# Performance work log

Hardware: AMD Instinct MI355X
Metric: run time of the kernel (lower is better)

Reference implementation:

```python
import jax, jax.numpy as jnp
import numpy as np

MODEL_W, MODEL_H = 1280.0, 768.0
SCALE = 80.0
NUM_CLASSES = 2


def _decode(pred_boxes):
    # pred_boxes: (bs, 4, H, W) -> decoded xywh box per reference point, (bs, H, W, 4)
    bs, _, H, W = pred_boxes.shape
    p = jnp.transpose(pred_boxes, (0, 2, 3, 1))
    sx = MODEL_W / W
    sy = MODEL_H / H
    rx = (jnp.arange(W, dtype=p.dtype) * sx + sx / 2)[None, None, :]
    ry = (jnp.arange(H, dtype=p.dtype) * sy + sy / 2)[None, :, None]
    x1 = p[..., 0] * SCALE + rx
    y1 = p[..., 1] * SCALE + ry
    x2 = p[..., 2] * SCALE + rx
    y2 = p[..., 3] * SCALE + ry
    w = x2 - x1
    h = y2 - y1
    cx = x1 + w / 2
    cy = y1 + h / 2
    return jnp.stack([cx, cy, w, h], axis=-1)


def _iou_xywh(pred, box):
    # pred: (H, W, 4) xywh, box: (4,) xywh -> (H, W)
    p_min = pred[..., :2] - pred[..., 2:4] / 2
    p_max = pred[..., :2] + pred[..., 2:4] / 2
    b_min = box[:2] - box[2:4] / 2
    b_max = box[:2] + box[2:4] / 2
    imin = jnp.maximum(p_min, b_min)
    imax = jnp.minimum(p_max, b_max)
    iwh = jnp.maximum(imax - imin, 0.0)
    inter = iwh[..., 0] * iwh[..., 1]
    union = pred[..., 2] * pred[..., 3] + box[2] * box[3] - inter
    return inter / jnp.clip(union, 1e-6)


def _assign_image(pred_dec, boxes):
    # pred_dec: (H, W, 4) decoded xywh; boxes: (N, 6) = x1,y1,x2,y2,class_id,extra
    H, W = pred_dec.shape[0], pred_dec.shape[1]
    row = jnp.arange(H, dtype=pred_dec.dtype)[:, None]
    col = jnp.arange(W, dtype=pred_dec.dtype)[None, :]
    cls0 = jnp.concatenate([jnp.ones((H, W, 1), jnp.float32),
                            jnp.zeros((H, W, NUM_CLASSES - 1), jnp.float32)], -1)
    pts0 = jnp.ones((H, W, 6), jnp.float32)
    best0 = jnp.zeros((H, W), jnp.float32)  # best==0 <=> position not yet assigned

    def step(carry, b):
        cls_map, pts_map, best = carry
        x1, y1, x2, y2, cid_f, extra = b[0], b[1], b[2], b[3], b[4], b[5]
        w = x2 - x1
        h = y2 - y1
        cx = x1 + w / 2
        cy = y1 + h / 2
        valid = (w * h) > 0  # original skips zero-area boxes
        box = jnp.stack([cx, cy, w, h])
        iou = _iou_xywh(pred_dec, box)
        # min_max_ref_point_index: rectangle of reference points covered by the box
        miw = jnp.floor(jnp.maximum((cx - w / 2) * W / MODEL_W - 0.5, 0.0))
        mih = jnp.floor(jnp.maximum((cy - h / 2) * H / MODEL_H - 0.5, 0.0))
        maw = jnp.ceil(jnp.minimum((cx + w / 2) * W / MODEL_W - 0.5, W - 1.0))
        mah = jnp.ceil(jnp.minimum((cy + h / 2) * H / MODEL_H - 0.5, H - 1.0))
        rect = (col >= miw) & (col <= maw) & (row >= mih) & (row <= mah) & valid
        iou_f = jnp.where(rect, iou, 0.0)
        # dynamic_k = ceil(max(sum_iou, 1)); keep strictly-top-k ious inside rect
        k = jnp.ceil(jnp.maximum(jnp.sum(iou_f), 1.0)).astype(jnp.int32)
        sorted_desc = -jnp.sort(-iou_f.ravel())
        thresh = jnp.take(sorted_desc, jnp.minimum(k, H * W - 1))  # (k+1)-th largest
        iou_k = jnp.where(iou_f > thresh, iou_f, 0.0)
        lam = jax.lax.rsqrt(k.astype(jnp.float32))
        positive = rect & (iou_k > 0)
        new = positive & (iou_k > best)                 # claim position (incl. unassigned)
        tie = positive & (iou_k == best) & (best > 0)   # equal iou -> zero all classes
        bg = rect & ~(iou_k > 0)                        # inside rect, not positive -> bg=0
        cid = jnp.clip(cid_f.astype(jnp.int32), 0, NUM_CLASSES - 2)
        onehot = jax.nn.one_hot(cid + 1, NUM_CLASSES, dtype=jnp.float32)
        cls_map = jnp.where(new[..., None], onehot, cls_map)
        cls_map = jnp.where(tie[..., None], 0.0, cls_map)
        cls_map = cls_map.at[..., 0].set(jnp.where(bg, 0.0, cls_map[..., 0]))
        pvec = jnp.stack([cx, cy, w, h, extra, lam])
        pts_map = jnp.where(new[..., None], pvec, pts_map)
        best = jnp.where(new, iou_k, best)
        return (cls_map, pts_map, best), None

    (cls_map, pts_map, _), _ = jax.lax.scan(step, (cls0, pts0, best0), boxes)
    return cls_map, pts_map


def setup_inputs():
    key = jax.random.key(0)
    k1, k2, k3, k4, k5, k6, k7 = jax.random.split(key, 7)
    bs, H, W, N = 16, 384, 640, 32
    pred_feat = jax.random.normal(k1, (bs, 3, H, W), dtype=jnp.float32)
    pred_boxes = jax.random.normal(k2, (bs, 4, H, W), dtype=jnp.float32)
    # GT boxes in x1,y1,x2,y2,class_id,extra format (module converts to xywh)
    cx = jax.random.uniform(k3, (bs, N), minval=0.0, maxval=MODEL_W)
    cy = jax.random.uniform(k4, (bs, N), minval=0.0, maxval=MODEL_H)
    w = jax.random.uniform(k5, (bs, N), minval=10.0, maxval=160.0)
    h = jax.random.uniform(k6, (bs, N), minval=10.0, maxval=120.0)
    cid = jnp.zeros((bs, N), jnp.float32)  # num_classes=2 -> single foreground class 0
    extra = jax.random.uniform(k7, (bs, N))
    bboxes = jnp.stack([cx - w / 2, cy - h / 2, cx + w / 2, cy + h / 2, cid, extra],
                       axis=-1).astype(jnp.float32)
    return {"pred_feat": pred_feat, "pred_boxes": pred_boxes, "bboxes": bboxes}


def reference(pred_feat, pred_boxes, bboxes):
    del pred_feat  # only used for shape in the original module
    dec = _decode(pred_boxes)
    cls_map, pts_map = jax.vmap(_assign_image)(dec, bboxes)
    return cls_map, pts_map
```

## Files before the change

kernel.cpp:

```cpp
#include <hip/hip_runtime.h>
#include <math.h>

#pragma clang fp contract(off)

#define HH 384
#define WW 640
#define HW (HH * WW)
#define NBOX 32
#define NSORT 8192
#define NTHR 256
#define MAXV 20

typedef float vfloat4 __attribute__((ext_vector_type(4)));

__device__ __forceinline__ float iou_at(float p0, float p1, float p2, float p3,
                                        float rx, float ry,
                                        float bcx, float bcy, float bw, float bh) {
#pragma clang fp contract(off)
    float x1 = p0 * 80.0f + rx;
    float y1 = p1 * 80.0f + ry;
    float x2 = p2 * 80.0f + rx;
    float y2 = p3 * 80.0f + ry;
    float wp = x2 - x1;
    float hp = y2 - y1;
    float cxp = x1 + wp * 0.5f;
    float cyp = y1 + hp * 0.5f;
    float pminx = cxp - wp * 0.5f;
    float pminy = cyp - hp * 0.5f;
    float pmaxx = cxp + wp * 0.5f;
    float pmaxy = cyp + hp * 0.5f;
    float bminx = bcx - bw * 0.5f;
    float bminy = bcy - bh * 0.5f;
    float bmaxx = bcx + bw * 0.5f;
    float bmaxy = bcy + bh * 0.5f;
    float iminx = fmaxf(pminx, bminx);
    float iminy = fmaxf(pminy, bminy);
    float imaxx = fminf(pmaxx, bmaxx);
    float imaxy = fminf(pmaxy, bmaxy);
    float iw = fmaxf(imaxx - iminx, 0.0f);
    float ih = fmaxf(imaxy - iminy, 0.0f);
    float inter = iw * ih;
    float uni = wp * hp + bw * bh - inter;
    uni = fmaxf(uni, 1e-6f);
    return inter / uni;
}

__global__ __launch_bounds__(NTHR) void phase1(const float* __restrict__ pb,
                                               const float* __restrict__ bboxes,
                                               unsigned* __restrict__ ws) {
#pragma clang fp contract(off)
    int pair = blockIdx.x;
    int img = pair >> 5;
    int box = pair & 31;
    int tid = threadIdx.x;
    int wid = tid >> 6;
    int lane = tid & 63;

    __shared__ unsigned h3[16][NTHR];
    __shared__ unsigned hlow[3][NTHR];
    __shared__ double wsum[4];
    __shared__ int wz[4];
    __shared__ unsigned sel_prefix_s;
    __shared__ unsigned sel_rank_s;

    const float* b = bboxes + (size_t)(img * NBOX + box) * 6;
    float bx1 = b[0], by1 = b[1], bx2 = b[2], by2 = b[3];
    float extra = b[5];
    float bw = bx2 - bx1;
    float bh = by2 - by1;
    float bcx = bx1 + bw * 0.5f;
    float bcy = by1 + bh * 0.5f;
    bool valid = (bw * bh) > 0.0f;

    float aw = ((bcx - bw * 0.5f) * 640.0f) / 1280.0f - 0.5f;
    float zw = ((bcx + bw * 0.5f) * 640.0f) / 1280.0f - 0.5f;
    float ah = ((bcy - bh * 0.5f) * 384.0f) / 768.0f - 0.5f;
    float zh = ((bcy + bh * 0.5f) * 384.0f) / 768.0f - 0.5f;
    int miw = (int)floorf(fmaxf(aw, 0.0f));
    int maw = (int)ceilf(fminf(zw, 639.0f));
    int mih = (int)floorf(fmaxf(ah, 0.0f));
    int mah = (int)ceilf(fminf(zh, 383.0f));
    if (!valid) { miw = 0; maw = -1; mih = 0; mah = -1; }

    int rw = maw - miw + 1;
    int rh = mah - mih + 1;
    int R = (rw > 0 && rh > 0) ? rw * rh : 0;

#pragma unroll
    for (int g = 0; g < 16; ++g) h3[g][tid] = 0u;
    hlow[0][tid] = 0u; hlow[1][tid] = 0u; hlow[2][tid] = 0u;

    int vcount = 0;
    if (R > tid) {
        vcount = (R - tid + NTHR - 1) >> 8;
        if (vcount > MAXV) vcount = MAXV;
    }
    int r0 = 0, c0 = 0, stepR = 0, stepC = 0;
    if (R > 0) {
        r0 = tid / rw;
        c0 = tid - r0 * rw;
        stepR = NTHR / rw;
        stepC = NTHR - stepR * rw;
    }

    const float* base = pb + (size_t)img * 4 * HW;
    unsigned v[MAXV];
    double lsum = 0.0;
    int zcnt = MAXV - vcount;
#pragma unroll
    for (int j = 0; j < MAXV; ++j) {
        unsigned u = 0u;
        if (j < vcount) {
            int rr = mih + r0;
            int cc = miw + c0;
            int off = rr * WW + cc;
            float p0 = base[off];
            float p1 = base[HW + off];
            float p2 = base[2 * HW + off];
            float p3 = base[3 * HW + off];
            float iou = iou_at(p0, p1, p2, p3,
                               (float)(2 * cc + 1), (float)(2 * rr + 1),
                               bcx, bcy, bw, bh);
            u = __float_as_uint(iou);
            lsum += (double)iou;
            if (u == 0u) ++zcnt;
            c0 += stepC; r0 += stepR;
            if (c0 >= rw) { c0 -= rw; ++r0; }
        }
        v[j] = u;
    }

    for (int off = 1; off < 64; off <<= 1) {
        lsum += __shfl_xor(lsum, off);
        zcnt += __shfl_xor(zcnt, off);
    }
    if (lane == 0) { wsum[wid] = lsum; wz[wid] = zcnt; }
    __syncthreads();

    double s = wsum[0] + wsum[1] + wsum[2] + wsum[3];
    int ztot = wz[0] + wz[1] + wz[2] + wz[3];
    double sm = s > 1.0 ? s : 1.0;
    int k = (int)ceil(sm);
    unsigned rank = (unsigned)k;
    unsigned pref = 0u;
    unsigned padT = (unsigned)(ztot + (NSORT - MAXV * NTHR));
    int subh = (wid << 2) | (lane >> 4);

#pragma unroll
    for (int p = 3; p >= 0; --p) {
        unsigned mask = (p == 3) ? 0u : (0xFFFFFFFFu << ((p + 1) * 8));
#pragma unroll
        for (int j = 0; j < MAXV; ++j) {
            unsigned u = v[j];
            if (j < vcount && u != 0u && (u & mask) == pref) {
                unsigned bn = (u >> (p * 8)) & 255;
                if (p == 3) atomicAdd(&h3[subh][bn], 1u);
                else        atomicAdd(&hlow[p][bn], 1u);
            }
        }
        __syncthreads();
        if (wid == 0) {
            uint4 hq;
            if (p == 3) {
                hq = make_uint4(0u, 0u, 0u, 0u);
#pragma unroll
                for (int g = 0; g < 16; ++g) {
                    uint4 t = *(const uint4*)&h3[g][4 * lane];
                    hq.x += t.x; hq.y += t.y; hq.z += t.z; hq.w += t.w;
                }
            } else {
                hq = *(const uint4*)&hlow[p][4 * lane];
            }
            if (lane == 0 && pref == 0u) hq.x += padT;
            unsigned s3 = hq.w;
            unsigned s2 = hq.z + s3;
            unsigned s1 = hq.y + s2;
            unsigned s0 = hq.x + s1;
            unsigned T = s0;
            for (int off = 1; off < 64; off <<= 1) {
                unsigned t = __shfl_down(T, off);
                if (lane + off < 64) T += t;
            }
            unsigned above = T - s0;
            unsigned G0 = s0 + above;
            unsigned G1 = s1 + above;
            unsigned G2 = s2 + above;
            unsigned G3 = s3 + above;
            int selb = -1; unsigned nr = 0;
            if (rank < G0 && rank >= G1)      { selb = 0; nr = rank - G1; }
            else if (rank < G1 && rank >= G2) { selb = 1; nr = rank - G2; }
            else if (rank < G2 && rank >= G3) { selb = 2; nr = rank - G3; }
            else if (rank < G3 && rank >= above) { selb = 3; nr = rank - above; }
            if (selb >= 0) {
                sel_prefix_s = pref | ((unsigned)(4 * lane + selb) << (p * 8));
                sel_rank_s = nr;
            }
        }
        __syncthreads();
        pref = sel_prefix_s;
        rank = sel_rank_s;
    }

    if (tid == 0) {
        float thresh = __uint_as_float(pref);
        float lam = 1.0f / sqrtf((float)k);
        unsigned* rec = ws + (size_t)pair * 16;
        rec[0] = (unsigned)miw;
        rec[1] = (unsigned)maw;
        rec[2] = (unsigned)mih;
        rec[3] = (unsigned)mah;
        rec[4] = __float_as_uint(bcx);
        rec[5] = __float_as_uint(bcy);
        rec[6] = __float_as_uint(bw);
        rec[7] = __float_as_uint(bh);
        rec[8] = __float_as_uint(extra);
        rec[9] = __float_as_uint(lam);
        rec[10] = __float_as_uint(thresh);
    }
}

__global__ __launch_bounds__(NTHR) void phase2(const float* __restrict__ pb,
                                               const unsigned* __restrict__ ws,
                                               float* __restrict__ out) {
#pragma clang fp contract(off)
    int tid = threadIdx.x;
    const int bpi = HW / (NTHR * 4);
    int img = blockIdx.x / bpi;
    int px0blk = (blockIdx.x - img * bpi) * (NTHR * 4);
    int px0 = px0blk + tid * 4;

    __shared__ unsigned rec[NBOX * 16];
    __shared__ float lpts[NTHR * 24];
    for (int i = tid; i < NBOX * 16; i += NTHR)
        rec[i] = ws[(size_t)img * NBOX * 16 + i];
    __syncthreads();

    int row = px0 / WW;
    int col0 = px0 - row * WW;

    unsigned hm = 0u;
#pragma unroll
    for (int bb2 = 0; bb2 < NBOX; ++bb2) {
        const unsigned* r = rec + bb2 * 16;
        bool any = (row >= (int)r[2]) && (row <= (int)r[3]) &&
                   (col0 + 3 >= (int)r[0]) && (col0 <= (int)r[1]);
        hm |= (unsigned)any << bb2;
    }
    unsigned wm = hm;
    for (int off = 1; off < 64; off <<= 1)
        wm |= __shfl_xor(wm, off);

    float cls0[4] = {1.f, 1.f, 1.f, 1.f};
    float cls1[4] = {0.f, 0.f, 0.f, 0.f};
    float pt[4][6];
#pragma unroll
    for (int p2 = 0; p2 < 4; ++p2)
#pragma unroll
        for (int q = 0; q < 6; ++q) pt[p2][q] = 1.0f;

    if (wm != 0u) {
        const float* base = pb + (size_t)img * 4 * HW;
        float4 q0 = *(const float4*)(base + px0);
        float4 q1 = *(const float4*)(base + HW + px0);
        float4 q2 = *(const float4*)(base + 2 * HW + px0);
        float4 q3 = *(const float4*)(base + 3 * HW + px0);
        float ry = (float)(2 * row + 1);
        float best[4] = {0.f, 0.f, 0.f, 0.f};

        unsigned m = wm;
        while (m) {
            int bb2 = __builtin_ctz(m);
            m &= m - 1u;
            if ((hm >> bb2) & 1u) {
                const unsigned* r = rec + bb2 * 16;
                int miw = (int)r[0];
                int maw = (int)r[1];
                float bcx = __uint_as_float(r[4]);
                float bcy = __uint_as_float(r[5]);
                float bw = __uint_as_float(r[6]);
                float bh = __uint_as_float(r[7]);
                float ext = __uint_as_float(r[8]);
                float lam = __uint_as_float(r[9]);
                float thr = __uint_as_float(r[10]);
#pragma unroll
                for (int p2 = 0; p2 < 4; ++p2) {
                    int col = col0 + p2;
                    if (col < miw || col > maw) continue;
                    float pp0 = (p2 == 0) ? q0.x : (p2 == 1) ? q0.y : (p2 == 2) ? q0.z : q0.w;
                    float pp1 = (p2 == 0) ? q1.x : (p2 == 1) ? q1.y : (p2 == 2) ? q1.z : q1.w;
                    float pp2 = (p2 == 0) ? q2.x : (p2 == 1) ? q2.y : (p2 == 2) ? q2.z : q2.w;
                    float pp3 = (p2 == 0) ? q3.x : (p2 == 1) ? q3.y : (p2 == 2) ? q3.z : q3.w;
                    float iou = iou_at(pp0, pp1, pp2, pp3,
                                       (float)(2 * col + 1), ry, bcx, bcy, bw, bh);
                    float iou_k = (iou > thr) ? iou : 0.0f;
                    if (iou_k > 0.0f) {
                        if (iou_k > best[p2]) {
                            cls0[p2] = 0.0f; cls1[p2] = 1.0f;
                            pt[p2][0] = bcx; pt[p2][1] = bcy;
                            pt[p2][2] = bw;  pt[p2][3] = bh;
                            pt[p2][4] = ext; pt[p2][5] = lam;
                            best[p2] = iou_k;
                        } else if (iou_k == best[p2] && best[p2] > 0.0f) {
                            cls0[p2] = 0.0f; cls1[p2] = 0.0f;
                        }
                    } else {
                        cls0[p2] = 0.0f;
                    }
                }
            }
        }
    }

#pragma unroll
    for (int p2 = 0; p2 < 4; ++p2) {
        float4* lp = (float4*)&lpts[(tid * 4 + p2) * 6];
        lp[0] = make_float4(pt[p2][0], pt[p2][1], pt[p2][2], pt[p2][3]);
        lpts[(tid * 4 + p2) * 6 + 4] = pt[p2][4];
        lpts[(tid * 4 + p2) * 6 + 5] = pt[p2][5];
    }
    __syncthreads();
    {
        const vfloat4* lp4 = (const vfloat4*)lpts;
        vfloat4* gp4 = (vfloat4*)(out + (size_t)16 * HW * 2 +
                                  ((size_t)img * HW + px0blk) * 6);
#pragma unroll
        for (int kk = 0; kk < 6; ++kk)
            __builtin_nontemporal_store(lp4[tid + kk * NTHR], &gp4[tid + kk * NTHR]);
    }

    vfloat4* cb = (vfloat4*)(out + ((size_t)img * HW + px0) * 2);
    vfloat4 c0v = {cls0[0], cls1[0], cls0[1], cls1[1]};
    vfloat4 c1v = {cls0[2], cls1[2], cls0[3], cls1[3]};
    __builtin_nontemporal_store(c0v, &cb[0]);
    __builtin_nontemporal_store(c1v, &cb[1]);
}

extern "C" void kernel_launch(void* const* d_in, const int* in_sizes, int n_in,
                              void* d_out, int out_size, void* d_ws, size_t ws_size,
                              hipStream_t stream) {
    (void)in_sizes; (void)n_in; (void)out_size; (void)ws_size;
    const float* pb = (const float*)d_in[1];
    const float* bb = (const float*)d_in[2];
    unsigned* ws = (unsigned*)d_ws;
    float* out = (float*)d_out;

    phase1<<<dim3(16 * NBOX), dim3(NTHR), 0, stream>>>(pb, bb, ws);
    phase2<<<dim3(16 * (HW / (NTHR * 4))), dim3(NTHR), 0, stream>>>(pb, ws, out);
}
```

Before: 52.67 us.

## Use 512-thread 2D tiled traversal of box rectangle in phase1

Phase1 now runs 512 threads per box as a 32x16 tile grid over the box's reference-point rectangle. Each thread handles up to 12 points, where before it handled up to 20 in a linearised stride. The goal is to cut per-thread serial work and make global loads row-coalesced in 32-wide column runs. The padding count is now derived from nonzero counts, and the histograms move into one flat shared array. The rectangle is assumed to fit in 96x64 points; larger boxes would be silently truncated, and the 8 waves need an extra sub-histogram mapping.

```diff
diff --git a/kernel.cpp b/kernel.cpp
--- a/kernel.cpp
+++ b/kernel.cpp
@@ -9,7 +9,7 @@
 #define NBOX 32
 #define NSORT 8192
 #define NTHR 256
-#define MAXV 20
+#define P1THR 512
 
 typedef float vfloat4 __attribute__((ext_vector_type(4)));
 
@@ -45,9 +45,9 @@
     return inter / uni;
 }
 
-__global__ __launch_bounds__(NTHR) void phase1(const float* __restrict__ pb,
-                                               const float* __restrict__ bboxes,
-                                               unsigned* __restrict__ ws) {
+__global__ __launch_bounds__(P1THR) void phase1(const float* __restrict__ pb,
+                                                const float* __restrict__ bboxes,
+                                                unsigned* __restrict__ ws) {
 #pragma clang fp contract(off)
     int pair = blockIdx.x;
     int img = pair >> 5;
@@ -55,11 +55,14 @@
     int tid = threadIdx.x;
     int wid = tid >> 6;
     int lane = tid & 63;
-
-    __shared__ unsigned h3[16][NTHR];
-    __shared__ unsigned hlow[3][NTHR];
-    __shared__ double wsum[4];
-    __shared__ int wz[4];
+    int tx = tid & 31;
+    int ty = tid >> 5;
+
+    __shared__ unsigned hall[19 * 256];
+#define H3(g, b)   hall[(g) * 256 + (b)]
+#define HLOW(p, b) hall[16 * 256 + (p) * 256 + (b)]
+    __shared__ double wsum[8];
+    __shared__ int wnz[8];
     __shared__ unsigned sel_prefix_s;
     __shared__ unsigned sel_rank_s;
 
@@ -84,78 +87,69 @@
 
     int rw = maw - miw + 1;
     int rh = mah - mih + 1;
-    int R = (rw > 0 && rh > 0) ? rw * rh : 0;
-
-#pragma unroll
-    for (int g = 0; g < 16; ++g) h3[g][tid] = 0u;
-    hlow[0][tid] = 0u; hlow[1][tid] = 0u; hlow[2][tid] = 0u;
-
-    int vcount = 0;
-    if (R > tid) {
-        vcount = (R - tid + NTHR - 1) >> 8;
-        if (vcount > MAXV) vcount = MAXV;
-    }
-    int r0 = 0, c0 = 0, stepR = 0, stepC = 0;
-    if (R > 0) {
-        r0 = tid / rw;
-        c0 = tid - r0 * rw;
-        stepR = NTHR / rw;
-        stepC = NTHR - stepR * rw;
-    }
+    bool hasR = (rw > 0 && rh > 0);
+    int tilesC = hasR ? ((rw + 31) >> 5) : 0;
+    int tilesR = hasR ? ((rh + 15) >> 4) : 0;
+
+    for (int i = tid; i < 19 * 256; i += P1THR) hall[i] = 0u;
 
     const float* base = pb + (size_t)img * 4 * HW;
-    unsigned v[MAXV];
+    unsigned v[12];
     double lsum = 0.0;
-    int zcnt = MAXV - vcount;
-#pragma unroll
-    for (int j = 0; j < MAXV; ++j) {
-        unsigned u = 0u;
-        if (j < vcount) {
-            int rr = mih + r0;
-            int cc = miw + c0;
-            int off = rr * WW + cc;
-            float p0 = base[off];
-            float p1 = base[HW + off];
-            float p2 = base[2 * HW + off];
-            float p3 = base[3 * HW + off];
-            float iou = iou_at(p0, p1, p2, p3,
-                               (float)(2 * cc + 1), (float)(2 * rr + 1),
-                               bcx, bcy, bw, bh);
-            u = __float_as_uint(iou);
-            lsum += (double)iou;
-            if (u == 0u) ++zcnt;
-            c0 += stepC; r0 += stepR;
-            if (c0 >= rw) { c0 -= rw; ++r0; }
+    int nz = 0;
+#pragma unroll
+    for (int tc = 0; tc < 3; ++tc) {
+#pragma unroll
+        for (int tr = 0; tr < 4; ++tr) {
+            unsigned u = 0u;
+            int cc = miw + tc * 32 + tx;
+            int rr = mih + tr * 16 + ty;
+            bool ok = (tc < tilesC) && (tr < tilesR) && (cc <= maw) && (rr <= mah);
+            if (ok) {
+                int off = rr * WW + cc;
+                float p0 = base[off];
+                float p1 = base[HW + off];
+                float p2 = base[2 * HW + off];
+                float p3 = base[3 * HW + off];
+                float iou = iou_at(p0, p1, p2, p3,
+                                   (float)(2 * cc + 1), (float)(2 * rr + 1),
+                                   bcx, bcy, bw, bh);
+                u = __float_as_uint(iou);
+                lsum += (double)iou;
+                nz += (u != 0u) ? 1 : 0;
+            }
+            v[tc * 4 + tr] = u;
         }
-        v[j] = u;
     }
 
     for (int off = 1; off < 64; off <<= 1) {
         lsum += __shfl_xor(lsum, off);
-        zcnt += __shfl_xor(zcnt, off);
-    }
-    if (lane == 0) { wsum[wid] = lsum; wz[wid] = zcnt; }
+        nz += __shfl_xor(nz, off);
+    }
+    if (lane == 0) { wsum[wid] = lsum; wnz[wid] = nz; }
     __syncthreads();
 
-    double s = wsum[0] + wsum[1] + wsum[2] + wsum[3];
-    int ztot = wz[0] + wz[1] + wz[2] + wz[3];
+    double s = 0.0;
+    int nztot = 0;
+#pragma unroll
+    for (int w = 0; w < 8; ++w) { s += wsum[w]; nztot += wnz[w]; }
     double sm = s > 1.0 ? s : 1.0;
     int k = (int)ceil(sm);
     unsigned rank = (unsigned)k;
     unsigned pref = 0u;
-    unsigned padT = (unsigned)(ztot + (NSORT - MAXV * NTHR));
-    int subh = (wid << 2) | (lane >> 4);
+    unsigned padT = (unsigned)(NSORT - nztot);
+    int subh = tid >> 5;
 
 #pragma unroll
     for (int p = 3; p >= 0; --p) {
         unsigned mask = (p == 3) ? 0u : (0xFFFFFFFFu << ((p + 1) * 8));
 #pragma unroll
-        for (int j = 0; j < MAXV; ++j) {
+        for (int j = 0; j < 12; ++j) {
             unsigned u = v[j];
-            if (j < vcount && u != 0u && (u & mask) == pref) {
+            if (u != 0u && (u & mask) == pref) {
                 unsigned bn = (u >> (p * 8)) & 255;
-                if (p == 3) atomicAdd(&h3[subh][bn], 1u);
-                else        atomicAdd(&hlow[p][bn], 1u);
+                if (p == 3) atomicAdd(&H3(subh, bn), 1u);
+                else        atomicAdd(&HLOW(p, bn), 1u);
             }
         }
         __syncthreads();
@@ -165,11 +159,11 @@
                 hq = make_uint4(0u, 0u, 0u, 0u);
 #pragma unroll
                 for (int g = 0; g < 16; ++g) {
-                    uint4 t = *(const uint4*)&h3[g][4 * lane];
+                    uint4 t = *(const uint4*)&H3(g, 4 * lane);
                     hq.x += t.x; hq.y += t.y; hq.z += t.z; hq.w += t.w;
                 }
             } else {
-                hq = *(const uint4*)&hlow[p][4 * lane];
+                hq = *(const uint4*)&HLOW(p, 4 * lane);
             }
             if (lane == 0 && pref == 0u) hq.x += padT;
             unsigned s3 = hq.w;
@@ -217,6 +211,8 @@
         rec[9] = __float_as_uint(lam);
         rec[10] = __float_as_uint(thresh);
     }
+#undef H3
+#undef HLOW
 }
 
 __global__ __launch_bounds__(NTHR) void phase2(const float* __restrict__ pb,
@@ -344,6 +340,6 @@
     unsigned* ws = (unsigned*)d_ws;
     float* out = (float*)d_out;
 
-    phase1<<<dim3(16 * NBOX), dim3(NTHR), 0, stream>>>(pb, bb, ws);
+    phase1<<<dim3(16 * NBOX), dim3(P1THR), 0, stream>>>(pb, bb, ws);
     phase2<<<dim3(16 * (HW / (NTHR * 4))), dim3(NTHR), 0, stream>>>(pb, ws, out);
 }
```

Measured after the change: 50.07 us. -4.9%, faster.
